# Performance work log

Measured on AMD Instinct MI355X. Metric: run time of the kernel, lower is better.

## Reference

```python
import jax, jax.numpy as jnp
import numpy as np

HEADS = 16
EPS = 1e-6


def _rms_norm(x, g):
    # RMSNorm computed in fp32 (matches torch x.float())
    xf = x.astype(jnp.float32)
    y = xf * jax.lax.rsqrt(jnp.mean(xf * xf, axis=-1, keepdims=True) + EPS)
    return y.astype(x.dtype) * g


def setup_inputs() -> dict:
    key = jax.random.key(0)
    ks = jax.random.split(key, 6)
    b, n, dim, emb_dim = 4, 2048, 2048, 2048
    d_head = dim // HEADS
    return {
        "x": jax.random.normal(ks[0], (b, n, dim), jnp.float32),
        "emb": jax.random.normal(ks[1], (b, 1, emb_dim), jnp.float32),
        "W_emb": jax.random.normal(ks[2], (emb_dim, 2 * dim), jnp.float32) * (emb_dim ** -0.5),
        "b_emb": jnp.zeros((2 * dim,), jnp.float32),
        "g_norm": jnp.ones((dim,), jnp.float32),
        "W_qkv": jax.random.normal(ks[3], (dim, 3 * dim), jnp.float32) * (dim ** -0.5),
        "g_q": jnp.ones((d_head,), jnp.float32),
        "g_k": jnp.ones((d_head,), jnp.float32),
        "W_out": jax.random.normal(ks[4], (dim, dim), jnp.float32) * (dim ** -0.5),
    }


def reference(x, emb, W_emb, b_emb, g_norm, W_qkv, g_q, g_k, W_out):
    b, n, dim = x.shape
    h = HEADS
    d = dim // h
    # AdaLN conditioning: RMSNorm(x) * (1 + scale) + shift
    scale_shift = emb @ W_emb + b_emb            # [b, 1, 2*dim]
    scale, shift = jnp.split(scale_shift, 2, axis=-1)
    xn = _rms_norm(x, g_norm) * (1.0 + scale) + shift
    # fused QKV projection then split to heads
    qkv = xn @ W_qkv                             # [b, n, 3*dim]
    qkv = qkv.reshape(b, n, 3, h, d)
    q, k, v = jnp.moveaxis(qkv, 2, 0)            # each [b, n, h, d]
    q = jnp.swapaxes(q, 1, 2)                    # [b, h, n, d]
    k = jnp.swapaxes(k, 1, 2)
    v = jnp.swapaxes(v, 1, 2)
    # per-head QK RMSNorm
    q = _rms_norm(q, g_q)
    k = _rms_norm(k, g_k)
    # SDPA (no mask, default scale 1/sqrt(d))
    logits = jnp.einsum("bhqd,bhkd->bhqk", q, k) * (d ** -0.5)
    attn = jax.nn.softmax(logits, axis=-1)
    o = jnp.einsum("bhqk,bhkd->bhqd", attn, v)   # [b, h, n, d]
    o = jnp.swapaxes(o, 1, 2).reshape(b, n, dim)
    return o + o @ W_out
```

## Files before the change

kernel.cpp:

```cpp
#include <hip/hip_runtime.h>
#include <stdint.h>

typedef unsigned short u16;
typedef __bf16 bf16x8 __attribute__((ext_vector_type(8)));
typedef float  f32x4  __attribute__((ext_vector_type(4)));

#define HEADS 16
#define DIM   2048
#define DHEAD 128
#define SEQ   2048
#define QKVN  (3*DIM)

__device__ __forceinline__ float bf2f(u16 u){
  union { unsigned int i; float f; } c; c.i = ((unsigned int)u) << 16; return c.f;
}
__device__ __forceinline__ u16 f2bf(float f){
  union { float f; unsigned int i; } c; c.f = f;
  unsigned int r = c.i + 0x7fffu + ((c.i >> 16) & 1u);
  return (u16)(r >> 16);
}

__device__ __forceinline__ void gl_lds16(const u16* g, u16* l){
  __builtin_amdgcn_global_load_lds((const __attribute__((address_space(1))) void*)g,
                                   (__attribute__((address_space(3))) void*)l,
                                   16, 0, 0);
}

__global__ void k_probe(const u16* __restrict__ w, int* __restrict__ flag){
  int i = threadIdx.x;
  u16 u = w[(size_t)i*131072];
  float v = bf2f(u);
  float a = fabsf(v);
  int wild = (a >= 1e4f) || (a > 0.f && a < 1e-4f) || (v != v);
  #pragma unroll
  for (int off=1;off<64;off<<=1) wild += __shfl_xor(wild, off, 64);
  if (i==0) *flag = (wild >= 32) ? 1 : 0;
}

__global__ __launch_bounds__(256) void k_sentinel1000(u16* __restrict__ out){
  size_t base = ((size_t)blockIdx.x*256 + threadIdx.x)*8;
  uint4 w; w.x=w.y=w.z=w.w=0x447A447Au;
  *(uint4*)(out + base) = w;
}
__global__ __launch_bounds__(256) void k_sentinel500(const int* __restrict__ flag, u16* __restrict__ out){
  if (*flag) return;
  size_t base = ((size_t)blockIdx.x*256 + threadIdx.x)*8;
  uint4 w; w.x=w.y=w.z=w.w=0x43FA43FAu;
  *(uint4*)(out + base) = w;
}

__global__ __launch_bounds__(256) void k_transpose_f(const int* __restrict__ flag,
                                                     const float* __restrict__ src, u16* __restrict__ dst,
                                                     int R, int C){
  if (!*flag) return;
  __shared__ u16 t[64][65];
  int tid = threadIdx.x;
  int c0 = blockIdx.x*64, r0 = blockIdx.y*64;
  #pragma unroll
  for (int i=0;i<16;++i){
    int idx = tid + i*256; int r = idx>>6, c = idx&63;
    t[r][c] = f2bf(src[(size_t)(r0+r)*C + c0 + c]);
  }
  __syncthreads();
  #pragma unroll
  for (int i=0;i<16;++i){
    int idx = tid + i*256; int r = idx>>6, c = idx&63;
    dst[(size_t)(c0+r)*R + r0 + c] = t[c][r];
  }
}

__global__ __launch_bounds__(256) void k_scale_shift(const int* __restrict__ flag,
                                                     const float* __restrict__ emb, const float* __restrict__ W,
                                                     const float* __restrict__ bias, float* __restrict__ ss){
  if (!*flag) return;
  __shared__ float eL[4*2048];
  int tid = threadIdx.x;
  for (int i=tid;i<4*2048;i+=256) eL[i] = emb[i];
  __syncthreads();
  int col = blockIdx.x*256 + tid;
  float a0=0,a1=0,a2=0,a3=0;
  for (int k=0;k<2048;++k){
    float w = W[(size_t)k*4096 + col];
    a0 += eL[k]*w; a1 += eL[2048+k]*w; a2 += eL[4096+k]*w; a3 += eL[6144+k]*w;
  }
  float bb = bias[col];
  ss[col]=a0+bb; ss[4096+col]=a1+bb; ss[8192+col]=a2+bb; ss[12288+col]=a3+bb;
}

__global__ __launch_bounds__(256) void k_rmsnorm_mod(const int* __restrict__ flag,
                                                     const float* __restrict__ x, const float* __restrict__ ss,
                                                     const float* __restrict__ g, u16* __restrict__ xn){
  if (!*flag) return;
  int row = blockIdx.x, tid = threadIdx.x;
  int b = row >> 11;
  const float* xr = x + (size_t)row*DIM;
  float4 v0 = ((const float4*)xr)[tid*2];
  float4 v1 = ((const float4*)xr)[tid*2+1];
  float xf[8] = {v0.x,v0.y,v0.z,v0.w,v1.x,v1.y,v1.z,v1.w};
  float s = 0.f;
  #pragma unroll
  for (int j=0;j<8;++j) s += xf[j]*xf[j];
  #pragma unroll
  for (int off=1;off<64;off<<=1) s += __shfl_xor(s, off, 64);
  __shared__ float red[4];
  if ((tid&63)==0) red[tid>>6] = s;
  __syncthreads();
  float tot = red[0]+red[1]+red[2]+red[3];
  float rs = rsqrtf(tot*(1.f/2048.f) + 1e-6f);
  const float* sb = ss + b*4096;
  unsigned int o[4];
  #pragma unroll
  for (int j=0;j<4;++j){
    int c0 = tid*8 + j*2;
    float y0 = xf[j*2]  *rs*g[c0]   * (1.f + sb[c0])   + sb[2048+c0];
    float y1 = xf[j*2+1]*rs*g[c0+1] * (1.f + sb[c0+1]) + sb[2048+c0+1];
    o[j] = (unsigned int)f2bf(y0) | ((unsigned int)f2bf(y1)<<16);
  }
  uint4 ov; ov.x=o[0]; ov.y=o[1]; ov.z=o[2]; ov.w=o[3];
  *(uint4*)&xn[(size_t)row*DIM + tid*8] = ov;
}

__global__ __launch_bounds__(256) void k_qk_norm(const int* __restrict__ flag,
                                                 u16* __restrict__ qkv, const float* __restrict__ gq,
                                                 const float* __restrict__ gk){
  if (!*flag) return;
  int tid=threadIdx.x, lane=tid&63, wv=tid>>6;
  unsigned int gid = blockIdx.x*4 + wv;
  int s = (int)(gid >> 17);
  unsigned int rr = gid & 131071u;
  unsigned int bn = rr >> 4; int head = (int)(rr & 15u);
  u16* p = qkv + (size_t)bn*QKVN + s*DIM + head*DHEAD + lane*2;
  unsigned int vv = *(const unsigned int*)p;
  float e0 = bf2f((u16)(vv&0xffffu)), e1 = bf2f((u16)(vv>>16));
  float sum = e0*e0 + e1*e1;
  #pragma unroll
  for (int off=1;off<64;off<<=1) sum += __shfl_xor(sum, off, 64);
  float rs = rsqrtf(sum*(1.f/128.f) + 1e-6f);
  const float* g = s ? gk : gq;
  float g0 = g[lane*2], g1 = g[lane*2+1];
  unsigned int o0 = f2bf(e0*rs*g0), o1 = f2bf(e1*rs*g1);
  *(unsigned int*)p = o0 | (o1<<16);
}

__global__ __launch_bounds__(256) void k_gemm_bt(const int* __restrict__ flag,
                                                 const u16* __restrict__ A, const u16* __restrict__ Bt,
                                                 void* __restrict__ Cv, const u16* __restrict__ addsrc,
                                                 int M, int N, int K, int outf32){
  if (!*flag) return;
  __shared__ __align__(16) u16 As[128*64];
  __shared__ __align__(16) u16 Bs[128*64];
  int tid = threadIdx.x, lane = tid&63, wv = tid>>6;
  int l15 = lane&15, qd = lane>>4;
  int swz = l15&7;

  int gx = gridDim.x, gy = gridDim.y;
  int nwg = gx*gy;
  int lin = blockIdx.y*gx + blockIdx.x;
  int sid = (nwg & 7) ? lin : ((lin & 7)*(nwg>>3) + (lin>>3));
  int bx = sid % gx, by = sid / gx;

  int row0 = by*128, col0 = bx*128;
  int wm = (wv&1)*64, wn = (wv>>1)*64;
  f32x4 acc[4][4];
  #pragma unroll
  for (int mt=0;mt<4;++mt)
    #pragma unroll
    for (int nt=0;nt<4;++nt) acc[mt][nt] = (f32x4){0.f,0.f,0.f,0.f};

  int r8 = tid>>3;
  int s8 = tid&7;

  for (int k0=0;k0<K;k0+=64){
    #pragma unroll
    for (int i=0;i<4;++i){
      int r = i*32 + r8;
      int kslot = s8 ^ (r&7);
      gl_lds16(A  + (size_t)(row0 + r)*K + k0 + kslot*8, &As[i*2048 + wv*512]);
      gl_lds16(Bt + (size_t)(col0 + r)*K + k0 + kslot*8, &Bs[i*2048 + wv*512]);
    }
    __syncthreads();
    #pragma unroll
    for (int ks=0;ks<2;++ks){
      bf16x8 af[4], bfr[4];
      #pragma unroll
      for (int mt=0;mt<4;++mt)
        af[mt]  = *(const bf16x8*)&As[(wm+mt*16+l15)*64 + (((ks*4+qd) ^ swz)*8)];
      #pragma unroll
      for (int nt=0;nt<4;++nt)
        bfr[nt] = *(const bf16x8*)&Bs[(wn+nt*16+l15)*64 + (((ks*4+qd) ^ swz)*8)];
      #pragma unroll
      for (int mt=0;mt<4;++mt)
        #pragma unroll
        for (int nt=0;nt<4;++nt)
          acc[mt][nt] = __builtin_amdgcn_mfma_f32_16x16x32_bf16(af[mt], bfr[nt], acc[mt][nt], 0,0,0);
    }
    __syncthreads();
  }
  #pragma unroll
  for (int mt=0;mt<4;++mt)
    #pragma unroll
    for (int nt=0;nt<4;++nt)
      #pragma unroll
      for (int r=0;r<4;++r){
        int row = row0 + wm + mt*16 + qd*4 + r;
        int col = col0 + wn + nt*16 + l15;
        float v = acc[mt][nt][r];
        if (addsrc) v += bf2f(addsrc[(size_t)row*N + col]);
        if (outf32) ((float*)Cv)[(size_t)row*N + col] = v;
        else        ((u16*)Cv)[(size_t)row*N + col] = f2bf(v);
      }
}

__global__ __launch_bounds__(256) void k_vtrans(const int* __restrict__ flag,
                                                const u16* __restrict__ qkv, u16* __restrict__ Vt){
  if (!*flag) return;
  __shared__ u16 t[64][66];
  int tid = threadIdx.x;
  int n0 = blockIdx.x*64, d0 = blockIdx.y*64, bh = blockIdx.z;
  int b = bh>>4, h = bh&15;
  #pragma unroll
  for (int i=0;i<2;++i){
    int idx = tid + i*256;
    int r = idx>>3, c8 = (idx&7)*8;
    uint4 v = *(const uint4*)(qkv + (size_t)(b*SEQ + n0 + r)*QKVN + 2*DIM + h*DHEAD + d0 + c8);
    const u16* pv = (const u16*)&v;
    #pragma unroll
    for (int j=0;j<8;++j) t[r][c8+j] = pv[j];
  }
  __syncthreads();
  #pragma unroll
  for (int i=0;i<2;++i){
    int idx = tid + i*256;
    int dr = idx>>3, nc8 = (idx&7)*8;
    union { u16 s[8]; uint4 v; } u;
    #pragma unroll
    for (int j=0;j<8;++j) u.s[j] = t[nc8+j][dr];
    *(uint4*)(Vt + (size_t)(bh*DHEAD + d0 + dr)*SEQ + n0 + nc8) = u.v;
  }
}

#define KT 64
__global__ __launch_bounds__(256, 4) void k_attn_mfma(const int* __restrict__ flag,
                                                      const u16* __restrict__ qkv,
                                                      const u16* __restrict__ Vt,
                                                      u16* __restrict__ O){
  if (!*flag) return;
  __shared__ __align__(16) u16 Ks[KT*DHEAD];
  __shared__ __align__(16) u16 Vs[DHEAD*KT];
  __shared__ __align__(16) u16 Ps[4*16*KT];

  int tid = threadIdx.x;
  int w = tid>>6, lane = tid&63;
  int l15 = lane&15, qd = lane>>4;
  int swz = (l15&7)<<3;

  int bh = blockIdx.y; int b = bh>>4, h = bh&15;
  int q0 = blockIdx.x*64 + w*16;

  const u16* Qbase = qkv + (size_t)(b*SEQ + q0 + l15)*QKVN + h*DHEAD;
  bf16x8 qf[4];
  #pragma unroll
  for (int ks=0;ks<4;++ks) qf[ks] = *(const bf16x8*)(Qbase + ks*32 + qd*8);

  f32x4 o_acc[8];
  #pragma unroll
  for (int cf=0;cf<8;++cf) o_acc[cf] = (f32x4){0.f,0.f,0.f,0.f};
  float mrun[4], lrun[4];
  #pragma unroll
  for (int r=0;r<4;++r){ mrun[r] = -3e38f; lrun[r] = 0.f; }
  const float sc = 0.08838834764831845f;

  const u16* Kb0 = qkv + (size_t)b*SEQ*QKVN + DIM + h*DHEAD;
  const u16* Vb0 = Vt + (size_t)bh*DHEAD*SEQ;
  u16* Pw = &Ps[w*16*KT];

  int rK0 = w*4 + (lane>>4), cK = lane&15;
  int rV0 = w*8 + (lane>>3), cV = lane&7;

  for (int kt0=0; kt0<SEQ; kt0+=KT){
    __syncthreads();
    #pragma unroll
    for (int i=0;i<4;++i){
      int rK = i*16 + rK0;
      gl_lds16(Kb0 + (size_t)(kt0 + rK)*QKVN + (cK ^ (rK&7))*8, &Ks[i*2048 + w*512]);
    }
    #pragma unroll
    for (int i=0;i<4;++i){
      int rV = i*32 + rV0;
      gl_lds16(Vb0 + (size_t)rV*SEQ + kt0 + (cV ^ (rV&7))*8, &Vs[i*2048 + w*512]);
    }
    __syncthreads();

    f32x4 s_acc[4];
    #pragma unroll
    for (int rf=0;rf<4;++rf) s_acc[rf] = (f32x4){0.f,0.f,0.f,0.f};
    __builtin_amdgcn_s_setprio(1);
    #pragma unroll
    for (int ks=0;ks<4;++ks){
      #pragma unroll
      for (int rf=0;rf<4;++rf){
        bf16x8 kb = *(const bf16x8*)&Ks[(rf*16+l15)*DHEAD + ((ks*32+qd*8) ^ swz)];
        s_acc[rf] = __builtin_amdgcn_mfma_f32_16x16x32_bf16(qf[ks], kb, s_acc[rf], 0,0,0);
      }
    }
    __builtin_amdgcn_s_setprio(0);

    float alpha[4], rs_[4];
    #pragma unroll
    for (int r=0;r<4;++r){
      float mx = fmaxf(fmaxf(s_acc[0][r], s_acc[1][r]), fmaxf(s_acc[2][r], s_acc[3][r]));
      #pragma unroll
      for (int off=1;off<16;off<<=1) mx = fmaxf(mx, __shfl_xor(mx, off, 64));
      float mnew = fmaxf(mrun[r], mx*sc);
      alpha[r] = __expf(mrun[r] - mnew);
      mrun[r] = mnew;
      rs_[r] = 0.f;
    }
    #pragma unroll
    for (int rf=0;rf<4;++rf){
      #pragma unroll
      for (int r=0;r<4;++r){
        float p = __expf(s_acc[rf][r]*sc - mrun[r]);
        u16 pb = f2bf(p);
        rs_[r] += bf2f(pb);
        int row = qd*4 + r;
        Pw[row*KT + ((rf*16+l15) ^ ((row&7)<<3))] = pb;
      }
    }
    #pragma unroll
    for (int r=0;r<4;++r){
      #pragma unroll
      for (int off=1;off<16;off<<=1) rs_[r] += __shfl_xor(rs_[r], off, 64);
      lrun[r] = lrun[r]*alpha[r] + rs_[r];
    }
    #pragma unroll
    for (int cf=0;cf<8;++cf){
      #pragma unroll
      for (int r=0;r<4;++r) o_acc[cf][r] *= alpha[r];
    }

    bf16x8 pf[2];
    #pragma unroll
    for (int ks=0;ks<2;++ks)
      pf[ks] = *(const bf16x8*)&Pw[l15*KT + ((ks*32+qd*8) ^ swz)];
    __builtin_amdgcn_s_setprio(1);
    #pragma unroll
    for (int ks=0;ks<2;++ks){
      #pragma unroll
      for (int cf=0;cf<8;++cf){
        bf16x8 vb = *(const bf16x8*)&Vs[(cf*16+l15)*KT + ((ks*32+qd*8) ^ swz)];
        o_acc[cf] = __builtin_amdgcn_mfma_f32_16x16x32_bf16(pf[ks], vb, o_acc[cf], 0,0,0);
      }
    }
    __builtin_amdgcn_s_setprio(0);
  }

  #pragma unroll
  for (int r=0;r<4;++r){
    float invl = 1.f / lrun[r];
    int qrow = q0 + qd*4 + r;
    u16* Orow = O + (size_t)(b*SEQ + qrow)*DIM + h*DHEAD;
    #pragma unroll
    for (int cf=0;cf<8;++cf)
      Orow[cf*16 + l15] = f2bf(o_acc[cf][r] * invl);
  }
}

extern "C" void kernel_launch(void* const* d_in, const int* in_sizes, int n_in,
                              void* d_out, int out_size, void* d_ws, size_t ws_size,
                              hipStream_t stream){
  const float* x      = (const float*)d_in[0];
  const float* emb    = (const float*)d_in[1];
  const float* W_emb  = (const float*)d_in[2];
  const float* b_emb  = (const float*)d_in[3];
  const float* g_norm = (const float*)d_in[4];
  const float* W_qkv  = (const float*)d_in[5];
  const float* g_q    = (const float*)d_in[6];
  const float* g_k    = (const float*)d_in[7];
  const float* W_out  = (const float*)d_in[8];

  const size_t REQUIRED = 167837952;
  if (ws_size < REQUIRED){
    k_sentinel1000<<<dim3(8192), dim3(256), 0, stream>>>((u16*)d_out);
    return;
  }

  char* ws = (char*)d_ws;
  size_t off = 0;
  int*   flag = (int*)(ws + off);  off += 256;
  float* ss   = (float*)(ws + off); off += (size_t)4*4096*4;
  u16* qkv    = (u16*)(ws + off);   off += (size_t)8192*6144*2;
  u16* WqkvT  = (u16*)(ws + off);   off += (size_t)6144*2048*2;
  u16* WoutT  = (u16*)(ws + off);   off += (size_t)2048*2048*2;
  u16* xn     = (u16*)(ws + off);   off += (size_t)8192*2048*2;
  u16* o_buf  = xn;
  u16* Vt     = (u16*)d_out;

  dim3 blk(256);
  k_probe      <<<dim3(1), dim3(64), 0, stream>>>((const u16*)d_in[5], flag);
  k_transpose_f<<<dim3(96,32),  blk, 0, stream>>>(flag, W_qkv, WqkvT, 2048, 6144);
  k_transpose_f<<<dim3(32,32),  blk, 0, stream>>>(flag, W_out, WoutT, 2048, 2048);
  k_scale_shift<<<dim3(16),     blk, 0, stream>>>(flag, emb, W_emb, b_emb, ss);
  k_rmsnorm_mod<<<dim3(8192),   blk, 0, stream>>>(flag, x, ss, g_norm, xn);
  k_gemm_bt    <<<dim3(48,64),  blk, 0, stream>>>(flag, xn, WqkvT, qkv, nullptr, 8192, 6144, 2048, 0);
  k_qk_norm    <<<dim3(65536),  blk, 0, stream>>>(flag, qkv, g_q, g_k);
  k_vtrans     <<<dim3(32,2,64),blk, 0, stream>>>(flag, qkv, Vt);
  k_attn_mfma  <<<dim3(32,64),  blk, 0, stream>>>(flag, qkv, Vt, o_buf);
  k_gemm_bt    <<<dim3(16,64),  blk, 0, stream>>>(flag, o_buf, WoutT, d_out, o_buf, 8192, 2048, 2048, 1);
  k_sentinel500<<<dim3(8192),   blk, 0, stream>>>(flag, (u16*)d_out);
}
```

Baseline: 1.049 ms.

## Process 32 query rows per wave in attention with transposed S and lazy rescale

Each wave now handles two 16-row query tiles, so every K/V tile loaded into LDS serves twice as many MFMAs, and the grid halves. The QK^T MFMA operands are swapped so each lane holds one query row's scores, which cuts the row max/sum reductions to two shuffles and lets P be written as packed 4-element stores. Output rescaling is skipped when the new max stays within a threshold of the running max (deferred rescale). The cost is more registers per thread (occupancy hint lowered from 4 to 3) and larger P scratch in LDS.

Measured after the change: 1.007 ms. 4.0% less time.

```diff
diff --git a/kernel.cpp b/kernel.cpp
--- a/kernel.cpp
+++ b/kernel.cpp
@@ -4,6 +4,7 @@
 typedef unsigned short u16;
 typedef __bf16 bf16x8 __attribute__((ext_vector_type(8)));
 typedef float  f32x4  __attribute__((ext_vector_type(4)));
+typedef unsigned short u16x4v __attribute__((ext_vector_type(4)));
 
 #define HEADS 16
 #define DIM   2048
@@ -240,14 +241,14 @@
 }
 
 #define KT 64
-__global__ __launch_bounds__(256, 4) void k_attn_mfma(const int* __restrict__ flag,
+__global__ __launch_bounds__(256, 3) void k_attn_mfma(const int* __restrict__ flag,
                                                       const u16* __restrict__ qkv,
                                                       const u16* __restrict__ Vt,
                                                       u16* __restrict__ O){
   if (!*flag) return;
   __shared__ __align__(16) u16 Ks[KT*DHEAD];
   __shared__ __align__(16) u16 Vs[DHEAD*KT];
-  __shared__ __align__(16) u16 Ps[4*16*KT];
+  __shared__ __align__(16) u16 Ps[4*32*KT];
 
   int tid = threadIdx.x;
   int w = tid>>6, lane = tid&63;
@@ -255,24 +256,25 @@
   int swz = (l15&7)<<3;
 
   int bh = blockIdx.y; int b = bh>>4, h = bh&15;
-  int q0 = blockIdx.x*64 + w*16;
-
-  const u16* Qbase = qkv + (size_t)(b*SEQ + q0 + l15)*QKVN + h*DHEAD;
-  bf16x8 qf[4];
-  #pragma unroll
-  for (int ks=0;ks<4;++ks) qf[ks] = *(const bf16x8*)(Qbase + ks*32 + qd*8);
-
-  f32x4 o_acc[8];
-  #pragma unroll
-  for (int cf=0;cf<8;++cf) o_acc[cf] = (f32x4){0.f,0.f,0.f,0.f};
-  float mrun[4], lrun[4];
-  #pragma unroll
-  for (int r=0;r<4;++r){ mrun[r] = -3e38f; lrun[r] = 0.f; }
+  int q0 = blockIdx.x*128 + w*32;
+
+  const u16* Qb = qkv + (size_t)(b*SEQ + q0 + l15)*QKVN + h*DHEAD;
+  bf16x8 qf0[4], qf1[4];
+  #pragma unroll
+  for (int ks=0;ks<4;++ks){
+    qf0[ks] = *(const bf16x8*)(Qb + ks*32 + qd*8);
+    qf1[ks] = *(const bf16x8*)(Qb + (size_t)16*QKVN + ks*32 + qd*8);
+  }
+
+  f32x4 o0[8], o1[8];
+  #pragma unroll
+  for (int cf=0;cf<8;++cf){ o0[cf] = (f32x4){0.f,0.f,0.f,0.f}; o1[cf] = (f32x4){0.f,0.f,0.f,0.f}; }
+  float mrun0=-3e38f, mrun1=-3e38f, lrun0=0.f, lrun1=0.f;
   const float sc = 0.08838834764831845f;
 
   const u16* Kb0 = qkv + (size_t)b*SEQ*QKVN + DIM + h*DHEAD;
   const u16* Vb0 = Vt + (size_t)bh*DHEAD*SEQ;
-  u16* Pw = &Ps[w*16*KT];
+  u16* Pw = &Ps[w*32*KT];
 
   int rK0 = w*4 + (lane>>4), cK = lane&15;
   int rV0 = w*8 + (lane>>3), cV = lane&7;
@@ -291,78 +293,99 @@
     }
     __syncthreads();
 
-    f32x4 s_acc[4];
-    #pragma unroll
-    for (int rf=0;rf<4;++rf) s_acc[rf] = (f32x4){0.f,0.f,0.f,0.f};
+    f32x4 s0[4], s1[4];
+    #pragma unroll
+    for (int rf=0;rf<4;++rf){ s0[rf] = (f32x4){0.f,0.f,0.f,0.f}; s1[rf] = (f32x4){0.f,0.f,0.f,0.f}; }
     __builtin_amdgcn_s_setprio(1);
     #pragma unroll
     for (int ks=0;ks<4;++ks){
       #pragma unroll
       for (int rf=0;rf<4;++rf){
         bf16x8 kb = *(const bf16x8*)&Ks[(rf*16+l15)*DHEAD + ((ks*32+qd*8) ^ swz)];
-        s_acc[rf] = __builtin_amdgcn_mfma_f32_16x16x32_bf16(qf[ks], kb, s_acc[rf], 0,0,0);
+        s0[rf] = __builtin_amdgcn_mfma_f32_16x16x32_bf16(kb, qf0[ks], s0[rf], 0,0,0);
+        s1[rf] = __builtin_amdgcn_mfma_f32_16x16x32_bf16(kb, qf1[ks], s1[rf], 0,0,0);
       }
     }
     __builtin_amdgcn_s_setprio(0);
 
-    float alpha[4], rs_[4];
-    #pragma unroll
-    for (int r=0;r<4;++r){
-      float mx = fmaxf(fmaxf(s_acc[0][r], s_acc[1][r]), fmaxf(s_acc[2][r], s_acc[3][r]));
-      #pragma unroll
-      for (int off=1;off<16;off<<=1) mx = fmaxf(mx, __shfl_xor(mx, off, 64));
-      float mnew = fmaxf(mrun[r], mx*sc);
-      alpha[r] = __expf(mrun[r] - mnew);
-      mrun[r] = mnew;
-      rs_[r] = 0.f;
-    }
+    float pm0 = -3e38f, pm1 = -3e38f;
+    #pragma unroll
+    for (int rf=0;rf<4;++rf)
+      #pragma unroll
+      for (int r=0;r<4;++r){
+        pm0 = fmaxf(pm0, s0[rf][r]);
+        pm1 = fmaxf(pm1, s1[rf][r]);
+      }
+    pm0 = fmaxf(pm0, __shfl_xor(pm0, 16, 64)); pm0 = fmaxf(pm0, __shfl_xor(pm0, 32, 64));
+    pm1 = fmaxf(pm1, __shfl_xor(pm1, 16, 64)); pm1 = fmaxf(pm1, __shfl_xor(pm1, 32, 64));
+    pm0 *= sc; pm1 *= sc;
+
+    int defer = __all(pm0 <= mrun0 + 8.f) & __all(pm1 <= mrun1 + 8.f);
+    if (!defer){
+      float mn0 = fmaxf(mrun0, pm0), mn1 = fmaxf(mrun1, pm1);
+      float a0 = __expf(mrun0 - mn0), a1 = __expf(mrun1 - mn1);
+      mrun0 = mn0; mrun1 = mn1;
+      lrun0 *= a0; lrun1 *= a1;
+      #pragma unroll
+      for (int r=0;r<4;++r){
+        int src = (lane & 48) | (qd*4 + r);
+        float ar0 = __shfl(a0, src, 64);
+        float ar1 = __shfl(a1, src, 64);
+        #pragma unroll
+        for (int cf=0;cf<8;++cf){ o0[cf][r] *= ar0; o1[cf][r] *= ar1; }
+      }
+    }
+
+    float rsum0 = 0.f, rsum1 = 0.f;
     #pragma unroll
     for (int rf=0;rf<4;++rf){
+      u16x4v pk0, pk1;
       #pragma unroll
       for (int r=0;r<4;++r){
-        float p = __expf(s_acc[rf][r]*sc - mrun[r]);
-        u16 pb = f2bf(p);
-        rs_[r] += bf2f(pb);
-        int row = qd*4 + r;
-        Pw[row*KT + ((rf*16+l15) ^ ((row&7)<<3))] = pb;
-      }
-    }
-    #pragma unroll
-    for (int r=0;r<4;++r){
-      #pragma unroll
-      for (int off=1;off<16;off<<=1) rs_[r] += __shfl_xor(rs_[r], off, 64);
-      lrun[r] = lrun[r]*alpha[r] + rs_[r];
-    }
-    #pragma unroll
-    for (int cf=0;cf<8;++cf){
-      #pragma unroll
-      for (int r=0;r<4;++r) o_acc[cf][r] *= alpha[r];
-    }
-
-    bf16x8 pf[2];
-    #pragma unroll
-    for (int ks=0;ks<2;++ks)
-      pf[ks] = *(const bf16x8*)&Pw[l15*KT + ((ks*32+qd*8) ^ swz)];
+        float e0 = __expf(s0[rf][r]*sc - mrun0); u16 pb0 = f2bf(e0); rsum0 += bf2f(pb0); pk0[r] = pb0;
+        float e1 = __expf(s1[rf][r]*sc - mrun1); u16 pb1 = f2bf(e1); rsum1 += bf2f(pb1); pk1[r] = pb1;
+      }
+      int cb = (rf*16 + qd*4) ^ swz;
+      *(u16x4v*)&Pw[l15*KT + cb]      = pk0;
+      *(u16x4v*)&Pw[(16+l15)*KT + cb] = pk1;
+    }
+    rsum0 += __shfl_xor(rsum0, 16, 64); rsum0 += __shfl_xor(rsum0, 32, 64);
+    rsum1 += __shfl_xor(rsum1, 16, 64); rsum1 += __shfl_xor(rsum1, 32, 64);
+    lrun0 += rsum0; lrun1 += rsum1;
+
+    bf16x8 pf0[2], pf1[2];
+    #pragma unroll
+    for (int ks=0;ks<2;++ks){
+      pf0[ks] = *(const bf16x8*)&Pw[l15*KT + ((ks*32+qd*8) ^ swz)];
+      pf1[ks] = *(const bf16x8*)&Pw[(16+l15)*KT + ((ks*32+qd*8) ^ swz)];
+    }
     __builtin_amdgcn_s_setprio(1);
     #pragma unroll
     for (int ks=0;ks<2;++ks){
       #pragma unroll
       for (int cf=0;cf<8;++cf){
         bf16x8 vb = *(const bf16x8*)&Vs[(cf*16+l15)*KT + ((ks*32+qd*8) ^ swz)];
-        o_acc[cf] = __builtin_amdgcn_mfma_f32_16x16x32_bf16(pf[ks], vb, o_acc[cf], 0,0,0);
+        o0[cf] = __builtin_amdgcn_mfma_f32_16x16x32_bf16(pf0[ks], vb, o0[cf], 0,0,0);
+        o1[cf] = __builtin_amdgcn_mfma_f32_16x16x32_bf16(pf1[ks], vb, o1[cf], 0,0,0);
       }
     }
     __builtin_amdgcn_s_setprio(0);
   }
 
+  float iv0 = 1.f / lrun0, iv1 = 1.f / lrun1;
   #pragma unroll
   for (int r=0;r<4;++r){
-    float invl = 1.f / lrun[r];
-    int qrow = q0 + qd*4 + r;
-    u16* Orow = O + (size_t)(b*SEQ + qrow)*DIM + h*DHEAD;
-    #pragma unroll
-    for (int cf=0;cf<8;++cf)
-      Orow[cf*16 + l15] = f2bf(o_acc[cf][r] * invl);
+    int src = (lane & 48) | (qd*4 + r);
+    float a0 = __shfl(iv0, src, 64);
+    float a1 = __shfl(iv1, src, 64);
+    int row0 = q0 + qd*4 + r;
+    u16* O0 = O + (size_t)(b*SEQ + row0)*DIM + h*DHEAD;
+    u16* O1 = O + (size_t)(b*SEQ + row0 + 16)*DIM + h*DHEAD;
+    #pragma unroll
+    for (int cf=0;cf<8;++cf){
+      O0[cf*16 + l15] = f2bf(o0[cf][r] * a0);
+      O1[cf*16 + l15] = f2bf(o1[cf][r] * a1);
+    }
   }
 }
 
@@ -405,7 +428,7 @@
   k_gemm_bt    <<<dim3(48,64),  blk, 0, stream>>>(flag, xn, WqkvT, qkv, nullptr, 8192, 6144, 2048, 0);
   k_qk_norm    <<<dim3(65536),  blk, 0, stream>>>(flag, qkv, g_q, g_k);
   k_vtrans     <<<dim3(32,2,64),blk, 0, stream>>>(flag, qkv, Vt);
-  k_attn_mfma  <<<dim3(32,64),  blk, 0, stream>>>(flag, qkv, Vt, o_buf);
+  k_attn_mfma  <<<dim3(16,64),  blk, 0, stream>>>(flag, qkv, Vt, o_buf);
   k_gemm_bt    <<<dim3(16,64),  blk, 0, stream>>>(flag, o_buf, WoutT, d_out, o_buf, 8192, 2048, 2048, 1);
   k_sentinel500<<<dim3(8192),   blk, 0, stream>>>(flag, (u16*)d_out);
 }
```
